# Optimization experiments

Measured on AMD Instinct MI355X. Metric: run time of the kernel, lower is better.

Reference implementation:

```python
import jax, jax.numpy as jnp
import numpy as np

BN_EPS = 1e-5
L2_EPS = 1e-12


def setup_inputs() -> dict:
    key = jax.random.key(0)
    k1, k2, k3 = jax.random.split(key, 3)
    B, N, D, K, G = 32, 2048, 512, 64, 16
    init_sc = 1.0 / np.sqrt(D)
    x = jax.random.normal(k1, (B, N, D), dtype=jnp.float32)
    clusters = init_sc * jax.random.normal(k2, (D, K + G), dtype=jnp.float32)
    clusters2 = init_sc * jax.random.normal(k3, (1, D, K), dtype=jnp.float32)
    bn_gamma = jnp.ones((K + G,), dtype=jnp.float32)
    bn_beta = jnp.zeros((K + G,), dtype=jnp.float32)
    return {"x": x, "clusters": clusters, "clusters2": clusters2,
            "bn_gamma": bn_gamma, "bn_beta": bn_beta}


def reference(x, clusters, clusters2, bn_gamma, bn_beta):
    B, N, D = x.shape
    K = clusters2.shape[-1]
    xf = x.reshape(B * N, D)
    # soft cluster assignment: [B*N, K+G]
    assn = xf @ clusters
    # BatchNorm1d (training-mode batch statistics, biased variance)
    mean = jnp.mean(assn, axis=0)
    var = jnp.var(assn, axis=0)
    assn = (assn - mean) * jax.lax.rsqrt(var + BN_EPS) * bn_gamma + bn_beta
    # softmax over clusters, then drop ghost clusters
    assn = jax.nn.softmax(assn, axis=1)[:, :K].reshape(B, N, K)
    # residual aggregation
    a_sum = jnp.sum(assn, axis=1, keepdims=True)          # [B, 1, K]
    a = a_sum * clusters2                                  # [B, D, K]
    vlad = jnp.einsum("bnk,bnd->bdk", assn, x) - a         # [B, D, K]
    # intra-normalization across feature dim D
    vlad = vlad / jnp.maximum(jnp.linalg.norm(vlad, axis=1, keepdims=True), L2_EPS)
    # flatten and global L2 normalization
    vlad = vlad.reshape(B, D * K)
    vlad = vlad / jnp.maximum(jnp.linalg.norm(vlad, axis=1, keepdims=True), L2_EPS)
    return vlad
```

## Files before the change

kernel.cpp:

```cpp
#include <hip/hip_runtime.h>
#include <hip/hip_bf16.h>
#include <stdint.h>

typedef __attribute__((ext_vector_type(8))) short short8;
typedef __attribute__((ext_vector_type(4))) float f32x4;

__device__ __forceinline__ float b2f(uint16_t u) {
  union { uint32_t i; float f; } v; v.i = ((uint32_t)u) << 16; return v.f;
}
__device__ __forceinline__ uint16_t f2b(float f) {
  uint32_t u = __float_as_uint(f);
  return (uint16_t)((u + 0x7FFFu + ((u >> 16) & 1u)) >> 16);
}
__device__ __forceinline__ uint32_t pk2(uint32_t lo, uint32_t hi) {
  return __builtin_amdgcn_perm(hi + 0x8000u, lo + 0x8000u, 0x07060302u);
}

__global__ __launch_bounds__(256) void k0_prep(const float* __restrict__ clusters,
                                               uint16_t* __restrict__ cB) {
  __shared__ float tile[32 * 80];
  const int kk = blockIdx.x, t = threadIdx.x;
#pragma unroll
  for (int i = t; i < 2560; i += 256) tile[i] = clusters[kk * 2560 + i];
  __syncthreads();
#pragma unroll
  for (int l = t; l < 2560; l += 256) {
    int i = l & 7, chunk = l >> 3;
    int lr = chunk & 15, q = (chunk >> 4) & 3, n = chunk >> 6;
    cB[kk * 2560 + l] = f2b(tile[(q * 8 + i) * 80 + n * 16 + lr]);
  }
}

__global__ __launch_bounds__(256) void k1_gemm1(
    const float* __restrict__ x, const uint16_t* __restrict__ cB,
    float* __restrict__ raw, float* __restrict__ part) {
  __shared__ float sf[1280];
  const int t = threadIdx.x;
  const int w = t >> 6, lane = t & 63, q = lane >> 4, lr = lane & 15;
  const int rbase = blockIdx.x * 128 + w * 32;

  f32x4 acc[2][5];
#pragma unroll
  for (int m = 0; m < 2; ++m)
#pragma unroll
    for (int n = 0; n < 5; ++n) acc[m][n] = 0.f;

  const float* xa = x + (size_t)(rbase + lr) * 512 + q * 8;
  const uint16_t* cq = cB + (size_t)(q * 16 + lr) * 8;

#pragma unroll 4
  for (int kk = 0; kk < 16; ++kk) {
    short8 a[2], bf[5];
#pragma unroll
    for (int m = 0; m < 2; ++m) {
      uint4 u0 = *(const uint4*)(xa + (size_t)m * 16 * 512 + kk * 32);
      uint4 u1 = *(const uint4*)(xa + (size_t)m * 16 * 512 + kk * 32 + 4);
      union { short8 s; uint32_t u[4]; } av;
      av.u[0] = pk2(u0.x, u0.y); av.u[1] = pk2(u0.z, u0.w);
      av.u[2] = pk2(u1.x, u1.y); av.u[3] = pk2(u1.z, u1.w);
      a[m] = av.s;
    }
#pragma unroll
    for (int n = 0; n < 5; ++n)
      bf[n] = *(const short8*)(cq + (size_t)(kk * 5 + n) * 512);
#pragma unroll
    for (int m = 0; m < 2; ++m)
#pragma unroll
      for (int n = 0; n < 5; ++n)
        acc[m][n] = __builtin_amdgcn_mfma_f32_16x16x32_bf16(a[m], bf[n], acc[m][n], 0, 0, 0);
  }

  float sums[5], sqs[5];
#pragma unroll
  for (int n = 0; n < 5; ++n) {
    float s = 0.f, qq = 0.f;
#pragma unroll
    for (int m = 0; m < 2; ++m) {
#pragma unroll
      for (int r = 0; r < 4; ++r) {
        float v = acc[m][n][r];
        s += v; qq += v * v;
        raw[(size_t)(rbase + m * 16 + q * 4 + r) * 80 + n * 16 + lr] = v;
      }
    }
    s += __shfl_xor(s, 16);  s += __shfl_xor(s, 32);
    qq += __shfl_xor(qq, 16); qq += __shfl_xor(qq, 32);
    sums[n] = s; sqs[n] = qq;
  }

  if (lane < 16) {
#pragma unroll
    for (int n = 0; n < 5; ++n) {
      sf[w * 160 + n * 16 + lr] = sums[n];
      sf[640 + w * 160 + n * 16 + lr] = sqs[n];
    }
  }
  __syncthreads();
  if (t < 160) {
    float a0 = sf[t] + sf[160 + t] + sf[320 + t] + sf[480 + t];
    float b0 = sf[640 + t] + sf[800 + t] + sf[960 + t] + sf[1120 + t];
    part[(size_t)blockIdx.x * 320 + t] = a0;
    part[(size_t)blockIdx.x * 320 + 160 + t] = b0;
  }
}

__global__ __launch_bounds__(64) void k2_stats(
    const float* __restrict__ part, const float* __restrict__ gamma,
    const float* __restrict__ beta, float* __restrict__ scsh,
    float* __restrict__ a_sum) {
  int c = blockIdx.x, t = threadIdx.x;
  int gid = c * 64 + t;
  if (gid < 2048) a_sum[gid] = 0.f;
  float s1 = 0.f, s2 = 0.f;
  for (int p = t; p < 512; p += 64) {
    s1 += part[(size_t)p * 320 + c];
    s2 += part[(size_t)p * 320 + 160 + c];
  }
#pragma unroll
  for (int o = 1; o < 64; o <<= 1) { s1 += __shfl_xor(s1, o); s2 += __shfl_xor(s2, o); }
  if (t == 0) {
    float mean = s1 * (1.f / 65536.f);
    float var = s2 * (1.f / 65536.f) - mean * mean;
    float sc = rsqrtf(var + 1e-5f) * gamma[c];
    scsh[c] = sc;
    scsh[80 + c] = beta[c] - mean * sc;
  }
}

__global__ __launch_bounds__(256) void k3_bnsoft(
    const float* __restrict__ raw, const float* __restrict__ scsh,
    uint16_t* __restrict__ pT, float* __restrict__ a_sum) {
  __shared__ float sc[80], sh[80];
  __shared__ __align__(16) uint16_t lpT[64 * 72];
  __shared__ float apart[256];
  const int t = threadIdx.x;
  if (t < 80) sc[t] = scsh[t];
  else if (t < 160) sh[t - 80] = scsh[t];
  __syncthreads();

  const int r = t >> 2, cg = t & 3;
  const float* rp = raw + ((size_t)blockIdx.x * 64 + r) * 80;
  const int cbase = cg * 20;

  float y[20];
#pragma unroll
  for (int j = 0; j < 20; j += 4) {
    float4 v = *(const float4*)(rp + cbase + j);
    y[j] = v.x; y[j + 1] = v.y; y[j + 2] = v.z; y[j + 3] = v.w;
  }
  float mx = -3.0e38f;
#pragma unroll
  for (int j = 0; j < 20; ++j) {
    int c = cbase + j;
    y[j] = y[j] * sc[c] + sh[c];
    mx = fmaxf(mx, y[j]);
  }
  mx = fmaxf(mx, __shfl_xor(mx, 1));
  mx = fmaxf(mx, __shfl_xor(mx, 2));
  float sum = 0.f;
#pragma unroll
  for (int j = 0; j < 20; ++j) { y[j] = __expf(y[j] - mx); sum += y[j]; }
  sum += __shfl_xor(sum, 1);
  sum += __shfl_xor(sum, 2);
  float inv = 1.0f / sum;
#pragma unroll
  for (int j = 0; j < 20; ++j) {
    int c = cbase + j;
    if (c < 64) lpT[c * 72 + r] = f2b(y[j] * inv);
  }
  __syncthreads();

  {
    int k = t >> 2, ng = t & 3;
    uint4 v0 = *(const uint4*)&lpT[k * 72 + ng * 16];
    uint4 v1 = *(const uint4*)&lpT[k * 72 + ng * 16 + 8];
    int b = blockIdx.x >> 5;
    int n0 = (blockIdx.x & 31) * 64;
    uint16_t* dst = pT + ((size_t)b * 64 + k) * 2048 + n0 + ng * 16;
    *(uint4*)dst = v0;
    *((uint4*)dst + 1) = v1;
    const uint16_t* pv = &lpT[k * 72 + ng * 16];
    float s = 0.f;
#pragma unroll
    for (int i = 0; i < 16; ++i) s += b2f(pv[i]);
    apart[k * 4 + ng] = s;
  }
  __syncthreads();
  if (t < 64) {
    float s = apart[t * 4] + apart[t * 4 + 1] + apart[t * 4 + 2] + apart[t * 4 + 3];
    atomicAdd(&a_sum[(blockIdx.x >> 5) * 64 + t], s);
  }
}

__global__ __launch_bounds__(256) void k4_gemm2(
    const float* __restrict__ x, const uint16_t* __restrict__ pT,
    float* __restrict__ vpart) {
  __shared__ __align__(16) uint16_t sx[2][64 * 40];
  __shared__ __align__(16) uint16_t sp[2][64 * 40];
  const int t = threadIdx.x;
  const int nb = blockIdx.x >> 8;
  const int b = (blockIdx.x >> 3) & 31;
  const int d0 = (blockIdx.x & 7) * 64;
  const int w = t >> 6, lane = t & 63, q = lane >> 4, lr = lane & 15;
  const int dl = w * 16 + lr;
  const int sw = ((dl >> 2) + (dl >> 4)) & 3;

  const int dd = t & 63, g = t >> 6;
  const int sg = ((dd >> 2) + (dd >> 4)) & 3;
  const int pk_ = t >> 2, pnq = t & 3;

  const float* xb = x + ((size_t)b * 2048 + (size_t)nb * 1024) * 512 + d0;
  const uint16_t* pb = pT + (size_t)b * 131072 + (size_t)nb * 1024;

  f32x4 acc[4];
#pragma unroll
  for (int j = 0; j < 4; ++j) acc[j] = 0.f;

  float xf[2][8];
  uint4 pf[2];

#define LOADC(c, si)                                                        \
  {                                                                         \
    const float* xc = xb + (size_t)(c) * 32 * 512;                          \
    _Pragma("unroll")                                                       \
    for (int jj = 0; jj < 8; ++jj)                                          \
      xf[si][jj] = xc[(size_t)(g * 8 + jj) * 512 + dd];                     \
    pf[si] = *(const uint4*)(pb + (size_t)pk_ * 2048 + (c) * 32 + pnq * 8); \
  }
#define STOREC(buf, si)                                                     \
  {                                                                         \
    uint16_t* xrow = &sx[buf][dd * 40 + (g ^ sg) * 8];                      \
    _Pragma("unroll")                                                       \
    for (int j = 0; j < 2; ++j) {                                           \
      *(uint32_t*)&xrow[j * 4] =                                            \
          pk2(__float_as_uint(xf[si][j * 4]), __float_as_uint(xf[si][j * 4 + 1])); \
      *(uint32_t*)&xrow[j * 4 + 2] =                                        \
          pk2(__float_as_uint(xf[si][j * 4 + 2]), __float_as_uint(xf[si][j * 4 + 3])); \
    }                                                                       \
    *(uint4*)&sp[buf][pk_ * 40 + pnq * 8] = pf[si];                         \
  }

  LOADC(0, 0)
  STOREC(0, 0)
  LOADC(1, 1)
  __syncthreads();

  for (int c = 0; c < 32; ++c) {
    const int cur = c & 1;
    if (c < 31) STOREC(cur ^ 1, (c + 1) & 1)
    if (c < 30) LOADC(c + 2, c & 1)
    const uint16_t* sxc = sx[cur];
    const uint16_t* spc = sp[cur];
    short8 af = *(const short8*)&sxc[dl * 40 + (q ^ sw) * 8];
#pragma unroll
    for (int j = 0; j < 4; ++j) {
      short8 bfj = *(const short8*)&spc[(j * 16 + lr) * 40 + q * 8];
      acc[j] = __builtin_amdgcn_mfma_f32_16x16x32_bf16(af, bfj, acc[j], 0, 0, 0);
    }
    __syncthreads();
  }
#undef LOADC
#undef STOREC

  float* vp = vpart + (size_t)nb * 1048576 + (size_t)b * 32768;
#pragma unroll
  for (int j = 0; j < 4; ++j)
#pragma unroll
    for (int r = 0; r < 4; ++r)
      vp[(size_t)(d0 + w * 16 + q * 4 + r) * 64 + j * 16 + lr] = acc[j][r];
}

__global__ __launch_bounds__(256) void k5a_ssq(
    const float* __restrict__ vpart, const float* __restrict__ a_sum,
    const float* __restrict__ c2, float* __restrict__ csq) {
  __shared__ float sred[256];
  const int t = threadIdx.x, b = blockIdx.x >> 4, dg = blockIdx.x & 15;
  const int k = t & 63, di = t >> 6;
  const float* v0 = vpart + (size_t)b * 32768;
  const float* v1 = v0 + 1048576;
  const float as = a_sum[b * 64 + k];
  float ssq = 0.f;
#pragma unroll
  for (int jj = 0; jj < 8; ++jj) {
    int i = (dg * 32 + di * 8 + jj) * 64 + k;
    float v = v0[i] + v1[i] - as * c2[i];
    ssq += v * v;
  }
  sred[di * 64 + k] = ssq;
  __syncthreads();
  if (t < 64) {
    csq[(size_t)blockIdx.x * 64 + t] =
        sred[t] + sred[64 + t] + sred[128 + t] + sred[192 + t];
  }
}

__global__ __launch_bounds__(64) void k5b_fin(
    const float* __restrict__ csq, float* __restrict__ linv,
    float* __restrict__ gscl) {
  const int t = threadIdx.x, b = blockIdx.x;
  float ssq = 0.f;
#pragma unroll
  for (int dg = 0; dg < 16; ++dg) ssq += csq[(size_t)(b * 16 + dg) * 64 + t];
  float iv = 1.0f / fmaxf(sqrtf(ssq), 1e-12f);
  linv[b * 64 + t] = iv;
  float contrib = ssq * iv * iv;
#pragma unroll
  for (int o = 1; o < 64; o <<= 1) contrib += __shfl_xor(contrib, o);
  if (t == 0) gscl[b] = 1.0f / fmaxf(sqrtf(contrib), 1e-12f);
}

__global__ __launch_bounds__(256) void k5c_norm(
    const float* __restrict__ vpart, const float* __restrict__ a_sum,
    const float* __restrict__ c2, const float* __restrict__ linv,
    const float* __restrict__ gscl, float* __restrict__ out) {
  __shared__ float lv[64], las[64];
  __shared__ float gs;
  const int t = threadIdx.x, b = blockIdx.x >> 4, seg = blockIdx.x & 15;
  if (t < 64) { lv[t] = linv[b * 64 + t]; las[t] = a_sum[b * 64 + t]; }
  if (t == 64) gs = gscl[b];
  __syncthreads();
  const float* v0 = vpart + (size_t)b * 32768;
  const float* v1 = v0 + 1048576;
  const float gg = gs;
#pragma unroll
  for (int u = 0; u < 2; ++u) {
    int i = seg * 2048 + u * 1024 + t * 4;
    int k0 = i & 63;
    float4 a = *(const float4*)(v0 + i);
    float4 bb = *(const float4*)(v1 + i);
    float4 cc = *(const float4*)(c2 + i);
    float4 o;
    o.x = (a.x + bb.x - las[k0 + 0] * cc.x) * lv[k0 + 0] * gg;
    o.y = (a.y + bb.y - las[k0 + 1] * cc.y) * lv[k0 + 1] * gg;
    o.z = (a.z + bb.z - las[k0 + 2] * cc.z) * lv[k0 + 2] * gg;
    o.w = (a.w + bb.w - las[k0 + 3] * cc.w) * lv[k0 + 3] * gg;
    *(float4*)&out[(size_t)b * 32768 + i] = o;
  }
}

extern "C" void kernel_launch(void* const* d_in, const int* in_sizes, int n_in,
                              void* d_out, int out_size, void* d_ws, size_t ws_size,
                              hipStream_t stream) {
  const float* x         = (const float*)d_in[0];
  const float* clusters  = (const float*)d_in[1];
  const float* clusters2 = (const float*)d_in[2];
  const float* gamma     = (const float*)d_in[3];
  const float* beta      = (const float*)d_in[4];
  float* out = (float*)d_out;
  char* ws = (char*)d_ws;

  uint16_t* cB = (uint16_t*)(ws + 0);
  float* part  = (float*)(ws + 81920);
  float* scsh  = (float*)(ws + 737280);
  float* a_sum = (float*)(ws + 737920);
  float* raw   = (float*)(ws + 746112);
  uint16_t* pT = (uint16_t*)(ws + 21717632);
  float* vpart = (float*)(ws + 30106240);
  float* csq   = (float*)(ws + 38494848);
  float* linv  = (float*)(ws + 38625920);
  float* gscl  = (float*)(ws + 38634112);

  hipLaunchKernelGGL(k0_prep,   dim3(16),  dim3(256), 0, stream, clusters, cB);
  hipLaunchKernelGGL(k1_gemm1,  dim3(512), dim3(256), 0, stream, x, cB, raw, part);
  hipLaunchKernelGGL(k2_stats,  dim3(80),  dim3(64),  0, stream, part, gamma, beta, scsh, a_sum);
  hipLaunchKernelGGL(k3_bnsoft, dim3(1024),dim3(256), 0, stream, raw, scsh, pT, a_sum);
  hipLaunchKernelGGL(k4_gemm2,  dim3(512), dim3(256), 0, stream, x, pT, vpart);
  hipLaunchKernelGGL(k5a_ssq,   dim3(512), dim3(256), 0, stream, vpart, a_sum, clusters2, csq);
  hipLaunchKernelGGL(k5b_fin,   dim3(32),  dim3(64),  0, stream, csq, linv, gscl);
  hipLaunchKernelGGL(k5c_norm,  dim3(512), dim3(256), 0, stream, vpart, a_sum, clusters2, linv, gscl, out);
}
```

Measured before the change: 261.0 us.

## Split gemm2 over four N-chunks with 64-row K-steps per stage

The second GEMM (assignment^T times x) now splits the N dimension into four chunks of 512 instead of two of 1024, doubling the grid to 1024 blocks. Each pipeline stage loads 64 rows instead of 32, so there are fewer sync iterations and two MFMA k-steps per stage, using larger LDS tiles. The normalization kernels now sum four partial results instead of two. This adds 8 MB of partial-result traffic and more per-thread registers in exchange for more parallelism and fewer barriers.

After: 275.0 us. 1.05x slower.

```diff
diff --git a/kernel.cpp b/kernel.cpp
--- a/kernel.cpp
+++ b/kernel.cpp
@@ -195,8 +195,8 @@
 __global__ __launch_bounds__(256) void k4_gemm2(
     const float* __restrict__ x, const uint16_t* __restrict__ pT,
     float* __restrict__ vpart) {
-  __shared__ __align__(16) uint16_t sx[2][64 * 40];
-  __shared__ __align__(16) uint16_t sp[2][64 * 40];
+  __shared__ __align__(16) uint16_t sx[2][64 * 72];
+  __shared__ __align__(16) uint16_t sp[2][64 * 72];
   const int t = threadIdx.x;
   const int nb = blockIdx.x >> 8;
   const int b = (blockIdx.x >> 3) & 31;
@@ -209,35 +209,35 @@
   const int sg = ((dd >> 2) + (dd >> 4)) & 3;
   const int pk_ = t >> 2, pnq = t & 3;
 
-  const float* xb = x + ((size_t)b * 2048 + (size_t)nb * 1024) * 512 + d0;
-  const uint16_t* pb = pT + (size_t)b * 131072 + (size_t)nb * 1024;
+  const float* xb = x + ((size_t)b * 2048 + (size_t)nb * 512) * 512 + d0;
+  const uint16_t* pb = pT + (size_t)b * 131072 + (size_t)nb * 512;
 
   f32x4 acc[4];
 #pragma unroll
   for (int j = 0; j < 4; ++j) acc[j] = 0.f;
 
-  float xf[2][8];
-  uint4 pf[2];
+  float xf[2][16];
+  uint4 pf[2][2];
 
 #define LOADC(c, si)                                                        \
   {                                                                         \
-    const float* xc = xb + (size_t)(c) * 32 * 512;                          \
+    const float* xc = xb + (size_t)(c) * 64 * 512;                          \
     _Pragma("unroll")                                                       \
-    for (int jj = 0; jj < 8; ++jj)                                          \
-      xf[si][jj] = xc[(size_t)(g * 8 + jj) * 512 + dd];                     \
-    pf[si] = *(const uint4*)(pb + (size_t)pk_ * 2048 + (c) * 32 + pnq * 8); \
+    for (int jj = 0; jj < 16; ++jj)                                         \
+      xf[si][jj] = xc[(size_t)(g * 16 + jj) * 512 + dd];                    \
+    pf[si][0] = *(const uint4*)(pb + (size_t)pk_ * 2048 + (c) * 64 + pnq * 16); \
+    pf[si][1] = *(const uint4*)(pb + (size_t)pk_ * 2048 + (c) * 64 + pnq * 16 + 8); \
   }
 #define STOREC(buf, si)                                                     \
   {                                                                         \
-    uint16_t* xrow = &sx[buf][dd * 40 + (g ^ sg) * 8];                      \
     _Pragma("unroll")                                                       \
-    for (int j = 0; j < 2; ++j) {                                           \
-      *(uint32_t*)&xrow[j * 4] =                                            \
-          pk2(__float_as_uint(xf[si][j * 4]), __float_as_uint(xf[si][j * 4 + 1])); \
-      *(uint32_t*)&xrow[j * 4 + 2] =                                        \
-          pk2(__float_as_uint(xf[si][j * 4 + 2]), __float_as_uint(xf[si][j * 4 + 3])); \
+    for (int j = 0; j < 16; j += 2) {                                       \
+      int u = g * 2 + (j >> 3);                                             \
+      *(uint32_t*)&sx[buf][dd * 72 + ((u ^ sg) * 8) + (j & 6)] =            \
+          pk2(__float_as_uint(xf[si][j]), __float_as_uint(xf[si][j + 1]));  \
     }                                                                       \
-    *(uint4*)&sp[buf][pk_ * 40 + pnq * 8] = pf[si];                         \
+    *(uint4*)&sp[buf][pk_ * 72 + pnq * 16] = pf[si][0];                     \
+    *(uint4*)&sp[buf][pk_ * 72 + pnq * 16 + 8] = pf[si][1];                 \
   }
 
   LOADC(0, 0)
@@ -245,17 +245,20 @@
   LOADC(1, 1)
   __syncthreads();
 
-  for (int c = 0; c < 32; ++c) {
+  for (int c = 0; c < 8; ++c) {
     const int cur = c & 1;
-    if (c < 31) STOREC(cur ^ 1, (c + 1) & 1)
-    if (c < 30) LOADC(c + 2, c & 1)
+    if (c < 7) STOREC(cur ^ 1, (c + 1) & 1)
+    if (c < 6) LOADC(c + 2, c & 1)
     const uint16_t* sxc = sx[cur];
     const uint16_t* spc = sp[cur];
-    short8 af = *(const short8*)&sxc[dl * 40 + (q ^ sw) * 8];
-#pragma unroll
-    for (int j = 0; j < 4; ++j) {
-      short8 bfj = *(const short8*)&spc[(j * 16 + lr) * 40 + q * 8];
-      acc[j] = __builtin_amdgcn_mfma_f32_16x16x32_bf16(af, bfj, acc[j], 0, 0, 0);
+#pragma unroll
+    for (int s = 0; s < 2; ++s) {
+      short8 af = *(const short8*)&sxc[dl * 72 + (s * 4 + (q ^ sw)) * 8];
+#pragma unroll
+      for (int j = 0; j < 4; ++j) {
+        short8 bfj = *(const short8*)&spc[(j * 16 + lr) * 72 + s * 32 + q * 8];
+        acc[j] = __builtin_amdgcn_mfma_f32_16x16x32_bf16(af, bfj, acc[j], 0, 0, 0);
+      }
     }
     __syncthreads();
   }
@@ -278,12 +281,14 @@
   const int k = t & 63, di = t >> 6;
   const float* v0 = vpart + (size_t)b * 32768;
   const float* v1 = v0 + 1048576;
+  const float* v2 = v0 + 2097152;
+  const float* v3 = v0 + 3145728;
   const float as = a_sum[b * 64 + k];
   float ssq = 0.f;
 #pragma unroll
   for (int jj = 0; jj < 8; ++jj) {
     int i = (dg * 32 + di * 8 + jj) * 64 + k;
-    float v = v0[i] + v1[i] - as * c2[i];
+    float v = (v0[i] + v1[i]) + (v2[i] + v3[i]) - as * c2[i];
     ssq += v * v;
   }
   sred[di * 64 + k] = ssq;
@@ -321,6 +326,8 @@
   __syncthreads();
   const float* v0 = vpart + (size_t)b * 32768;
   const float* v1 = v0 + 1048576;
+  const float* v2 = v0 + 2097152;
+  const float* v3 = v0 + 3145728;
   const float gg = gs;
 #pragma unroll
   for (int u = 0; u < 2; ++u) {
@@ -328,12 +335,14 @@
     int k0 = i & 63;
     float4 a = *(const float4*)(v0 + i);
     float4 bb = *(const float4*)(v1 + i);
+    float4 cc2 = *(const float4*)(v2 + i);
+    float4 dd2 = *(const float4*)(v3 + i);
     float4 cc = *(const float4*)(c2 + i);
     float4 o;
-    o.x = (a.x + bb.x - las[k0 + 0] * cc.x) * lv[k0 + 0] * gg;
-    o.y = (a.y + bb.y - las[k0 + 1] * cc.y) * lv[k0 + 1] * gg;
-    o.z = (a.z + bb.z - las[k0 + 2] * cc.z) * lv[k0 + 2] * gg;
-    o.w = (a.w + bb.w - las[k0 + 3] * cc.w) * lv[k0 + 3] * gg;
+    o.x = ((a.x + bb.x) + (cc2.x + dd2.x) - las[k0 + 0] * cc.x) * lv[k0 + 0] * gg;
+    o.y = ((a.y + bb.y) + (cc2.y + dd2.y) - las[k0 + 1] * cc.y) * lv[k0 + 1] * gg;
+    o.z = ((a.z + bb.z) + (cc2.z + dd2.z) - las[k0 + 2] * cc.z) * lv[k0 + 2] * gg;
+    o.w = ((a.w + bb.w) + (cc2.w + dd2.w) - las[k0 + 3] * cc.w) * lv[k0 + 3] * gg;
     *(float4*)&out[(size_t)b * 32768 + i] = o;
   }
 }
@@ -356,16 +365,16 @@
   float* raw   = (float*)(ws + 746112);
   uint16_t* pT = (uint16_t*)(ws + 21717632);
   float* vpart = (float*)(ws + 30106240);
-  float* csq   = (float*)(ws + 38494848);
-  float* linv  = (float*)(ws + 38625920);
-  float* gscl  = (float*)(ws + 38634112);
-
-  hipLaunchKernelGGL(k0_prep,   dim3(16),  dim3(256), 0, stream, clusters, cB);
-  hipLaunchKernelGGL(k1_gemm1,  dim3(512), dim3(256), 0, stream, x, cB, raw, part);
-  hipLaunchKernelGGL(k2_stats,  dim3(80),  dim3(64),  0, stream, part, gamma, beta, scsh, a_sum);
-  hipLaunchKernelGGL(k3_bnsoft, dim3(1024),dim3(256), 0, stream, raw, scsh, pT, a_sum);
-  hipLaunchKernelGGL(k4_gemm2,  dim3(512), dim3(256), 0, stream, x, pT, vpart);
-  hipLaunchKernelGGL(k5a_ssq,   dim3(512), dim3(256), 0, stream, vpart, a_sum, clusters2, csq);
-  hipLaunchKernelGGL(k5b_fin,   dim3(32),  dim3(64),  0, stream, csq, linv, gscl);
-  hipLaunchKernelGGL(k5c_norm,  dim3(512), dim3(256), 0, stream, vpart, a_sum, clusters2, linv, gscl, out);
-}
+  float* csq   = (float*)(ws + 46883456);
+  float* linv  = (float*)(ws + 47014528);
+  float* gscl  = (float*)(ws + 47022720);
+
+  hipLaunchKernelGGL(k0_prep,   dim3(16),   dim3(256), 0, stream, clusters, cB);
+  hipLaunchKernelGGL(k1_gemm1,  dim3(512),  dim3(256), 0, stream, x, cB, raw, part);
+  hipLaunchKernelGGL(k2_stats,  dim3(80),   dim3(64),  0, stream, part, gamma, beta, scsh, a_sum);
+  hipLaunchKernelGGL(k3_bnsoft, dim3(1024), dim3(256), 0, stream, raw, scsh, pT, a_sum);
+  hipLaunchKernelGGL(k4_gemm2,  dim3(1024), dim3(256), 0, stream, x, pT, vpart);
+  hipLaunchKernelGGL(k5a_ssq,   dim3(512),  dim3(256), 0, stream, vpart, a_sum, clusters2, csq);
+  hipLaunchKernelGGL(k5b_fin,   dim3(32),   dim3(64),  0, stream, csq, linv, gscl);
+  hipLaunchKernelGGL(k5c_norm,  dim3(512),  dim3(256), 0, stream, vpart, a_sum, clusters2, linv, gscl, out);
+}
```
